# Optimization experiments

Measured on AMD Instinct MI355X. Metric: run time of the kernel, lower is better.

## Reference

```python
import jax, jax.numpy as jnp
import numpy as np

HIDDEN = 4096
NUM_HEADS = 32
NUM_KV_HEADS = 8
HEAD_DIM = 128


def setup_inputs() -> dict:
    key = jax.random.key(0)
    k0, k1, k2, k3, k4 = jax.random.split(key, 5)
    B, S = 1, 2048
    s = 0.02
    return {
        "hidden_states": jax.random.normal(k0, (B, S, HIDDEN), dtype=jnp.float32),
        "Wq": jax.random.normal(k1, (HIDDEN, NUM_HEADS * HEAD_DIM), dtype=jnp.float32) * s,
        "Wk": jax.random.normal(k2, (HIDDEN, NUM_KV_HEADS * HEAD_DIM), dtype=jnp.float32) * s,
        "Wv": jax.random.normal(k3, (HIDDEN, NUM_KV_HEADS * HEAD_DIM), dtype=jnp.float32) * s,
        "Wo": jax.random.normal(k4, (NUM_HEADS * HEAD_DIM, HIDDEN), dtype=jnp.float32) * s,
    }


def reference(hidden_states, Wq, Wk, Wv, Wo):
    B, S, _ = hidden_states.shape
    n_rep = NUM_HEADS // NUM_KV_HEADS
    # Projections -> [B, H, S, D]
    q = (hidden_states @ Wq).reshape(B, S, NUM_HEADS, HEAD_DIM).transpose(0, 2, 1, 3)
    k = (hidden_states @ Wk).reshape(B, S, NUM_KV_HEADS, HEAD_DIM).transpose(0, 2, 1, 3)
    v = (hidden_states @ Wv).reshape(B, S, NUM_KV_HEADS, HEAD_DIM).transpose(0, 2, 1, 3)
    # GQA expansion: repeat_interleave KV heads to match query head count
    k = jnp.repeat(k, n_rep, axis=1)
    v = jnp.repeat(v, n_rep, axis=1)
    scale = HEAD_DIM ** -0.5
    # Full [B, H, S, S] attention scores (faithful to the naive reference)
    scores = jnp.einsum("bhqd,bhkd->bhqk", q, k) * scale
    causal = jnp.tril(jnp.ones((S, S), dtype=bool))
    scores = jnp.where(causal[None, None], scores, jnp.float32(-jnp.inf))
    probs = jax.nn.softmax(scores, axis=-1)
    out = jnp.einsum("bhqk,bhkd->bhqd", probs, v)
    out = out.transpose(0, 2, 1, 3).reshape(B, S, NUM_HEADS * HEAD_DIM)
    return out @ Wo
```

## Files before the change

kernel.cpp:

```cpp
#include <hip/hip_runtime.h>
#include <hip/hip_bf16.h>

typedef __bf16 bf16;
typedef __bf16 bf16x4 __attribute__((ext_vector_type(4)));
typedef __bf16 bf16x8 __attribute__((ext_vector_type(8)));
typedef float  f32x4  __attribute__((ext_vector_type(4)));

#define SEQ  2048
#define HID  4096
#define QKVN 6144

__device__ __forceinline__ void gload_lds16(const void* g, void* l) {
  __builtin_amdgcn_global_load_lds(
      (const __attribute__((address_space(1))) void*)g,
      (__attribute__((address_space(3))) void*)l, 16, 0, 0);
}

__global__ __launch_bounds__(256) void cast_f32_bf16(const float* __restrict__ in,
                                                     bf16* __restrict__ out, int n) {
  int i = (blockIdx.x * 256 + threadIdx.x) * 4;
  int stride = gridDim.x * 256 * 4;
  for (; i < n; i += stride) {
    float4 v = *(const float4*)(in + i);
    bf16x4 o;
    o[0] = (bf16)v.x; o[1] = (bf16)v.y; o[2] = (bf16)v.z; o[3] = (bf16)v.w;
    *(bf16x4*)(out + i) = o;
  }
}

__global__ __launch_bounds__(256) void transpose_cast(const float* __restrict__ W,
                                                      bf16* __restrict__ Wt,
                                                      int N, int roff) {
  __shared__ float tile[64][65];
  int k0 = blockIdx.y * 64;
  int n0 = blockIdx.x * 64;
  int t = threadIdx.x;
  int lr = t >> 4;
  int lc = (t & 15) * 4;
#pragma unroll
  for (int p = 0; p < 4; ++p) {
    int row = p * 16 + lr;
    float4 v = *(const float4*)(W + (size_t)(k0 + row) * N + n0 + lc);
    tile[row][lc] = v.x; tile[row][lc + 1] = v.y;
    tile[row][lc + 2] = v.z; tile[row][lc + 3] = v.w;
  }
  __syncthreads();
#pragma unroll
  for (int p = 0; p < 4; ++p) {
    int n = p * 16 + lr;
    bf16x4 o;
#pragma unroll
    for (int q = 0; q < 4; ++q) o[q] = (bf16)tile[lc + q][n];
    *(bf16x4*)(Wt + (size_t)(roff + n0 + n) * 4096 + k0 + lc) = o;
  }
}

__global__ __launch_bounds__(256) void transpose_v(const bf16* __restrict__ QKV,
                                                   bf16* __restrict__ Vt_g) {
  __shared__ bf16 tile[32][33];
  int s0 = blockIdx.x * 32;
  int d0 = blockIdx.y * 32;
  int g  = blockIdx.z;
  int t = threadIdx.x;
  int r = t >> 5, c = t & 31;
#pragma unroll
  for (int p = 0; p < 4; ++p)
    tile[r + p * 8][c] = QKV[(size_t)(s0 + r + p * 8) * QKVN + 5120 + g * 128 + d0 + c];
  __syncthreads();
#pragma unroll
  for (int p = 0; p < 4; ++p)
    Vt_g[(size_t)(g * 128 + d0 + r + p * 8) * SEQ + s0 + c] = tile[c][r + p * 8];
}

template <typename OUT_T>
__global__ __launch_bounds__(256) void gemm_bt(const bf16* __restrict__ A,
                                               const bf16* __restrict__ Bt,
                                               OUT_T* __restrict__ C,
                                               int K, int ldc) {
  __shared__ __align__(16) bf16 Abuf[128 * 64];
  __shared__ __align__(16) bf16 Bbuf[128 * 64];
  int m0 = blockIdx.y * 128, n0 = blockIdx.x * 128;
  int tid = threadIdx.x, w = tid >> 6, lane = tid & 63;
  int wr = w >> 1, wc = w & 1;
  int l15 = lane & 15, l4 = lane >> 4;
  f32x4 acc[4][4] = {};
  const int nk = K >> 6;
  for (int kt = 0; kt < nk; ++kt) {
    int k0 = kt << 6;
#pragma unroll
    for (int p = 0; p < 4; ++p) {
      int c = p * 256 + tid;
      int row = c >> 3, slot = c & 7;
      int ssl = (slot ^ (row & 7)) << 4;
      gload_lds16((const char*)(A + (size_t)(m0 + row) * K + k0) + ssl, (char*)Abuf + c * 16);
      gload_lds16((const char*)(Bt + (size_t)(n0 + row) * K + k0) + ssl, (char*)Bbuf + c * 16);
    }
    __syncthreads();
    bf16x8 af[4][2], bfr[4][2];
#pragma unroll
    for (int m = 0; m < 4; ++m)
#pragma unroll
      for (int kk = 0; kk < 2; ++kk) {
        int row = wr * 64 + m * 16 + l15;
        af[m][kk] = *(const bf16x8*)((const char*)Abuf + row * 128 +
                                     (((kk * 4 + l4) ^ (row & 7)) << 4));
      }
#pragma unroll
    for (int n = 0; n < 4; ++n)
#pragma unroll
      for (int kk = 0; kk < 2; ++kk) {
        int row = wc * 64 + n * 16 + l15;
        bfr[n][kk] = *(const bf16x8*)((const char*)Bbuf + row * 128 +
                                      (((kk * 4 + l4) ^ (row & 7)) << 4));
      }
#pragma unroll
    for (int kk = 0; kk < 2; ++kk)
#pragma unroll
      for (int m = 0; m < 4; ++m)
#pragma unroll
        for (int n = 0; n < 4; ++n)
          acc[m][n] = __builtin_amdgcn_mfma_f32_16x16x32_bf16(af[m][kk], bfr[n][kk],
                                                              acc[m][n], 0, 0, 0);
    __syncthreads();
  }
#pragma unroll
  for (int m = 0; m < 4; ++m)
#pragma unroll
    for (int n = 0; n < 4; ++n)
#pragma unroll
      for (int i = 0; i < 4; ++i) {
        int row = m0 + wr * 64 + m * 16 + l4 * 4 + i;
        int col = n0 + wc * 64 + n * 16 + l15;
        C[(size_t)row * ldc + col] = (OUT_T)acc[m][n][i];
      }
}

__global__ __launch_bounds__(256, 2) void attn_kernel(const bf16* __restrict__ QKV,
                                                      const bf16* __restrict__ Vt_g,
                                                      bf16* __restrict__ attn) {
  __shared__ __align__(16) bf16 Klds[2][64 * 128];
  __shared__ __align__(16) bf16 Vlds[2][64 * 128];
  __shared__ __align__(16) bf16 Plds[4 * 16 * 64];
  const int bid = blockIdx.x;
  const int g = bid & 7;
  const int rest = bid >> 3;
  const int hi = rest & 3;
  const int pair = rest >> 2;
  const int qb_a = pair, qb_b = 31 - pair;
  const int tid = threadIdx.x, w = tid >> 6, lane = tid & 63;
  const int h = g * 4 + hi;
  const int l15 = lane & 15, l4 = lane >> 4;
  const int wqA = qb_a * 64 + w * 16;
  const int wqB = qb_b * 64 + w * 16;
  const int qcol = h * 128;
  const int kcol = 4096 + g * 128;
  const float scale = 0.08838834764831845f;
  const float LOG2E = 1.4426950408889634f;

  const bf16* Vhead = Vt_g + (size_t)g * 128 * SEQ;

  bf16x8 aqA[4], aqB[4];
#pragma unroll
  for (int kc = 0; kc < 4; ++kc) {
    aqA[kc] = *(const bf16x8*)(QKV + (size_t)(wqA + l15) * QKVN + qcol + kc * 32 + l4 * 8);
    aqB[kc] = *(const bf16x8*)(QKV + (size_t)(wqB + l15) * QKVN + qcol + kc * 32 + l4 * 8);
  }

  f32x4 acc_oA[8] = {}, acc_oB[8] = {};
  float mA[4], lA[4], mB[4], lB[4];
#pragma unroll
  for (int i = 0; i < 4; ++i) { mA[i] = -1e30f; lA[i] = 0.f; mB[i] = -1e30f; lB[i] = 0.f; }

  auto stageKV = [&](int kb, int buf) {
#pragma unroll
    for (int j = 0; j < 4; ++j) {
      int c = tid + (j << 8);
      int krow = c >> 4, kslot = c & 15;
      gload_lds16((const char*)(QKV + (size_t)(kb + krow) * QKVN + kcol) +
                      ((kslot ^ (krow & 7)) << 4),
                  (char*)Klds[buf] + c * 16);
      int vrow = c >> 3, vslot = c & 7;
      gload_lds16(Vhead + (size_t)vrow * SEQ + kb + ((vslot ^ (vrow & 7)) << 3),
                  (char*)Vlds[buf] + c * 16);
    }
  };

  auto compute_block = [&](const bf16x8* aq, f32x4* acc_o, float* mrow, float* lrow,
                           int wq0, int kb, int cur) {
    const char* Kbuf = (const char*)Klds[cur];
    const char* Vbuf = (const char*)Vlds[cur];
    f32x4 accs[4] = {};
    __builtin_amdgcn_s_setprio(1);
#pragma unroll
    for (int n = 0; n < 4; ++n) {
      int row_ = n * 16 + l15;
      int sw = (row_ & 7) << 4;
#pragma unroll
      for (int kc = 0; kc < 4; ++kc) {
        bf16x8 bk = *(const bf16x8*)(Kbuf + row_ * 256 + ((kc * 64 + l4 * 16) ^ sw));
        accs[n] = __builtin_amdgcn_mfma_f32_16x16x32_bf16(aq[kc], bk, accs[n], 0, 0, 0);
      }
    }
    __builtin_amdgcn_s_setprio(0);
    bool needmask = (kb + 64 > wq0);
    float s[4][4];
#pragma unroll
    for (int n = 0; n < 4; ++n)
#pragma unroll
      for (int i = 0; i < 4; ++i) {
        float v = accs[n][i] * scale;
        if (needmask) {
          int ks = kb + n * 16 + l15;
          int qr = wq0 + l4 * 4 + i;
          if (ks > qr) v = -1e30f;
        }
        s[n][i] = v;
      }
    float t4[4];
#pragma unroll
    for (int i = 0; i < 4; ++i) {
      float t = fmaxf(fmaxf(s[0][i], s[1][i]), fmaxf(s[2][i], s[3][i]));
      t = fmaxf(t, __shfl_xor(t, 1));
      t = fmaxf(t, __shfl_xor(t, 2));
      t = fmaxf(t, __shfl_xor(t, 4));
      t = fmaxf(t, __shfl_xor(t, 8));
      t4[i] = t;
    }
    float dm = fmaxf(fmaxf(t4[0] - mrow[0], t4[1] - mrow[1]),
                     fmaxf(t4[2] - mrow[2], t4[3] - mrow[3]));
    if (!__all(dm <= 8.0f)) {
      float fac[4];
#pragma unroll
      for (int i = 0; i < 4; ++i) {
        float mnew = fmaxf(mrow[i], t4[i]);
        fac[i] = exp2f((mrow[i] - mnew) * LOG2E);
        mrow[i] = mnew;
        lrow[i] *= fac[i];
      }
#pragma unroll
      for (int n2 = 0; n2 < 8; ++n2)
#pragma unroll
        for (int i = 0; i < 4; ++i)
          acc_o[n2][i] *= fac[i];
    }
    float ps[4][4];
#pragma unroll
    for (int i = 0; i < 4; ++i) {
      float psum = 0.f;
#pragma unroll
      for (int n = 0; n < 4; ++n) {
        float p = exp2f((s[n][i] - mrow[i]) * LOG2E);
        ps[n][i] = p; psum += p;
      }
      psum += __shfl_xor(psum, 1);
      psum += __shfl_xor(psum, 2);
      psum += __shfl_xor(psum, 4);
      psum += __shfl_xor(psum, 8);
      lrow[i] += psum;
    }
    char* Pw = (char*)Plds + w * 2048;
#pragma unroll
    for (int n = 0; n < 4; ++n)
#pragma unroll
      for (int i = 0; i < 4; ++i) {
        int r = l4 * 4 + i;
        int b = (r * 128 + (n * 16 + l15) * 2) ^ ((r & 7) << 4);
        *(bf16*)(Pw + b) = (bf16)ps[n][i];
      }
    __builtin_amdgcn_sched_barrier(0);
    asm volatile("" ::: "memory");
    bf16x8 pa[2];
#pragma unroll
    for (int kc = 0; kc < 2; ++kc)
      pa[kc] = *(const bf16x8*)(Pw + (l15 * 128 + ((kc * 64 + l4 * 16) ^ ((l15 & 7) << 4))));
    __builtin_amdgcn_s_setprio(1);
#pragma unroll
    for (int n2 = 0; n2 < 8; ++n2) {
      int row_ = n2 * 16 + l15;
      int sw = (row_ & 7) << 4;
#pragma unroll
      for (int kc = 0; kc < 2; ++kc) {
        bf16x8 bv = *(const bf16x8*)(Vbuf + row_ * 128 + ((kc * 64 + l4 * 16) ^ sw));
        acc_o[n2] = __builtin_amdgcn_mfma_f32_16x16x32_bf16(pa[kc], bv, acc_o[n2], 0, 0, 0);
      }
    }
    __builtin_amdgcn_s_setprio(0);
    asm volatile("" ::: "memory");
  };

  stageKV(0, 0);
  __syncthreads();

  int cur = 0;
  for (int kbi = 0; kbi <= qb_b; ++kbi) {
    int kb = kbi * 64;
    if (kbi < qb_b) stageKV(kb + 64, cur ^ 1);
    if (kbi <= qb_a) compute_block(aqA, acc_oA, mA, lA, wqA, kb, cur);
    compute_block(aqB, acc_oB, mB, lB, wqB, kb, cur);
    __syncthreads();
    cur ^= 1;
  }

#pragma unroll
  for (int n2 = 0; n2 < 8; ++n2)
#pragma unroll
    for (int i = 0; i < 4; ++i) {
      int col = qcol + n2 * 16 + l15;
      attn[(size_t)(wqA + l4 * 4 + i) * 4096 + col] = (bf16)(acc_oA[n2][i] / lA[i]);
      attn[(size_t)(wqB + l4 * 4 + i) * 4096 + col] = (bf16)(acc_oB[n2][i] / lB[i]);
    }
}

extern "C" void kernel_launch(void* const* d_in, const int* in_sizes, int n_in,
                              void* d_out, int out_size, void* d_ws, size_t ws_size,
                              hipStream_t stream) {
  const float* X  = (const float*)d_in[0];
  const float* Wq = (const float*)d_in[1];
  const float* Wk = (const float*)d_in[2];
  const float* Wv = (const float*)d_in[3];
  const float* Wo = (const float*)d_in[4];
  float* out = (float*)d_out;

  const size_t XB_OFF  = 0;
  const size_t WT_OFF  = 16777216;
  const size_t VT_OFF  = WT_OFF + 33554432;
  const size_t QKV_OFF = 16777216 + 50331648;
  if (ws_size < (size_t)92274688) return;

  char* ws = (char*)d_ws;
  bf16* Xb    = (bf16*)(ws + XB_OFF);
  bf16* Wt    = (bf16*)(ws + WT_OFF);
  bf16* Vt_g  = (bf16*)(ws + VT_OFF);
  bf16* QKV   = (bf16*)(ws + QKV_OFF);
  bf16* attnb = Xb;

  cast_f32_bf16<<<2048, 256, 0, stream>>>(X, Xb, SEQ * HID);
  transpose_cast<<<dim3(4096 / 64, 4096 / 64), 256, 0, stream>>>(Wq, Wt, 4096, 0);
  transpose_cast<<<dim3(1024 / 64, 4096 / 64), 256, 0, stream>>>(Wk, Wt, 1024, 4096);
  transpose_cast<<<dim3(1024 / 64, 4096 / 64), 256, 0, stream>>>(Wv, Wt, 1024, 5120);
  gemm_bt<bf16><<<dim3(QKVN / 128, SEQ / 128), 256, 0, stream>>>(Xb, Wt, QKV, HID, QKVN);
  transpose_cast<<<dim3(4096 / 64, 4096 / 64), 256, 0, stream>>>(Wo, Wt, 4096, 0);
  transpose_v<<<dim3(SEQ / 32, 4, 8), 256, 0, stream>>>(QKV, Vt_g);
  attn_kernel<<<512, 256, 0, stream>>>(QKV, Vt_g, attnb);
  gemm_bt<float><<<dim3(4096 / 128, SEQ / 128), 256, 0, stream>>>(attnb, Wt, out, HID, 4096);
}
```

Baseline: 379.8 us.

## Rewrite attention inner loop with 32x32 MFMA and register-resident P

Switches the attention kernel from 16x16x32 to 32x32x16 bf16 MFMA and computes S transposed, with K as the A operand. The softmax probabilities are then packed into the PV operand in registers with v_cvt_pk_bf16_f32 and v_permlane32_swap, so the per-wave LDS round trip for P goes away. The work split also changes: each wave now owns 32 query rows of a single q-block, with two waves on the late block and two on the early block, instead of every wave handling 16 rows of both. K/V LDS swizzles are re-laid out to match the new fragments. The risks are more register pressure from the 16-wide accumulators and idle time for the early-block waves once their causal range is done.

```diff
diff --git a/kernel.cpp b/kernel.cpp
--- a/kernel.cpp
+++ b/kernel.cpp
@@ -5,6 +5,8 @@
 typedef __bf16 bf16x4 __attribute__((ext_vector_type(4)));
 typedef __bf16 bf16x8 __attribute__((ext_vector_type(8)));
 typedef float  f32x4  __attribute__((ext_vector_type(4)));
+typedef float  f32x16 __attribute__((ext_vector_type(16)));
+typedef unsigned u32x4 __attribute__((ext_vector_type(4)));
 
 #define SEQ  2048
 #define HID  4096
@@ -14,6 +16,15 @@
   __builtin_amdgcn_global_load_lds(
       (const __attribute__((address_space(1))) void*)g,
       (__attribute__((address_space(3))) void*)l, 16, 0, 0);
+}
+
+__device__ __forceinline__ unsigned cvtpk(float lo, float hi) {
+  unsigned r;
+  asm("v_cvt_pk_bf16_f32 %0, %1, %2" : "=v"(r) : "v"(lo), "v"(hi));
+  return r;
+}
+__device__ __forceinline__ void plswap(unsigned& a, unsigned& b) {
+  asm("v_permlane32_swap_b32 %0, %1" : "+v"(a), "+v"(b));
 }
 
 __global__ __launch_bounds__(256) void cast_f32_bf16(const float* __restrict__ in,
@@ -140,7 +151,6 @@
                                                       bf16* __restrict__ attn) {
   __shared__ __align__(16) bf16 Klds[2][64 * 128];
   __shared__ __align__(16) bf16 Vlds[2][64 * 128];
-  __shared__ __align__(16) bf16 Plds[4 * 16 * 64];
   const int bid = blockIdx.x;
   const int g = bid & 7;
   const int rest = bid >> 3;
@@ -148,144 +158,116 @@
   const int pair = rest >> 2;
   const int qb_a = pair, qb_b = 31 - pair;
   const int tid = threadIdx.x, w = tid >> 6, lane = tid & 63;
-  const int h = g * 4 + hi;
-  const int l15 = lane & 15, l4 = lane >> 4;
-  const int wqA = qb_a * 64 + w * 16;
-  const int wqB = qb_b * 64 + w * 16;
-  const int qcol = h * 128;
+  const int l31 = lane & 31, hh = lane >> 5;
+  const int head = g * 4 + hi;
+  const bool isB = (w < 2);
+  const int myqb = isB ? qb_b : qb_a;
+  const int unit_q0 = myqb * 64 + (w & 1) * 32;
+  const int qcol = head * 128;
   const int kcol = 4096 + g * 128;
   const float scale = 0.08838834764831845f;
   const float LOG2E = 1.4426950408889634f;
 
   const bf16* Vhead = Vt_g + (size_t)g * 128 * SEQ;
 
-  bf16x8 aqA[4], aqB[4];
-#pragma unroll
-  for (int kc = 0; kc < 4; ++kc) {
-    aqA[kc] = *(const bf16x8*)(QKV + (size_t)(wqA + l15) * QKVN + qcol + kc * 32 + l4 * 8);
-    aqB[kc] = *(const bf16x8*)(QKV + (size_t)(wqB + l15) * QKVN + qcol + kc * 32 + l4 * 8);
-  }
-
-  f32x4 acc_oA[8] = {}, acc_oB[8] = {};
-  float mA[4], lA[4], mB[4], lB[4];
-#pragma unroll
-  for (int i = 0; i < 4; ++i) { mA[i] = -1e30f; lA[i] = 0.f; mB[i] = -1e30f; lB[i] = 0.f; }
+  bf16x8 qf[8];
+#pragma unroll
+  for (int db = 0; db < 8; ++db)
+    qf[db] = *(const bf16x8*)(QKV + (size_t)(unit_q0 + l31) * QKVN + qcol +
+                              db * 16 + hh * 8);
+
+  f32x16 acc_o[4] = {};
+  float m_run = -1e30f, l_run = 0.f;
 
   auto stageKV = [&](int kb, int buf) {
 #pragma unroll
     for (int j = 0; j < 4; ++j) {
       int c = tid + (j << 8);
-      int krow = c >> 4, kslot = c & 15;
-      gload_lds16((const char*)(QKV + (size_t)(kb + krow) * QKVN + kcol) +
-                      ((kslot ^ (krow & 7)) << 4),
-                  (char*)Klds[buf] + c * 16);
-      int vrow = c >> 3, vslot = c & 7;
-      gload_lds16(Vhead + (size_t)vrow * SEQ + kb + ((vslot ^ (vrow & 7)) << 3),
-                  (char*)Vlds[buf] + c * 16);
+      int row = c >> 4, s = c & 15;
+      int sl = s ^ (row & 15);
+      gload_lds16((const char*)(QKV + (size_t)(kb + row) * QKVN + kcol) + (sl << 4),
+                  (char*)Klds[buf] + (c << 4));
+      int d = row * 2 + (sl >> 3);
+      int ko = (sl & 7) << 3;
+      gload_lds16(Vhead + (size_t)d * SEQ + kb + ko, (char*)Vlds[buf] + (c << 4));
     }
   };
 
-  auto compute_block = [&](const bf16x8* aq, f32x4* acc_o, float* mrow, float* lrow,
-                           int wq0, int kb, int cur) {
-    const char* Kbuf = (const char*)Klds[cur];
-    const char* Vbuf = (const char*)Vlds[cur];
-    f32x4 accs[4] = {};
+  auto compute_unit = [&](int kb, int cur) {
+    const char* Kb = (const char*)Klds[cur];
+    const char* Vb = (const char*)Vlds[cur];
+    f32x16 s0 = {}, s1 = {};
     __builtin_amdgcn_s_setprio(1);
 #pragma unroll
-    for (int n = 0; n < 4; ++n) {
-      int row_ = n * 16 + l15;
-      int sw = (row_ & 7) << 4;
-#pragma unroll
-      for (int kc = 0; kc < 4; ++kc) {
-        bf16x8 bk = *(const bf16x8*)(Kbuf + row_ * 256 + ((kc * 64 + l4 * 16) ^ sw));
-        accs[n] = __builtin_amdgcn_mfma_f32_16x16x32_bf16(aq[kc], bk, accs[n], 0, 0, 0);
-      }
+    for (int db = 0; db < 8; ++db) {
+      int slot = (db * 2 + hh) ^ (l31 & 15);
+      bf16x8 k0 = *(const bf16x8*)(Kb + l31 * 256 + slot * 16);
+      bf16x8 k1 = *(const bf16x8*)(Kb + (32 + l31) * 256 + slot * 16);
+      s0 = __builtin_amdgcn_mfma_f32_32x32x16_bf16(k0, qf[db], s0, 0, 0, 0);
+      s1 = __builtin_amdgcn_mfma_f32_32x32x16_bf16(k1, qf[db], s1, 0, 0, 0);
     }
     __builtin_amdgcn_s_setprio(0);
-    bool needmask = (kb + 64 > wq0);
-    float s[4][4];
-#pragma unroll
-    for (int n = 0; n < 4; ++n)
-#pragma unroll
-      for (int i = 0; i < 4; ++i) {
-        float v = accs[n][i] * scale;
-        if (needmask) {
-          int ks = kb + n * 16 + l15;
-          int qr = wq0 + l4 * 4 + i;
-          if (ks > qr) v = -1e30f;
-        }
-        s[n][i] = v;
-      }
-    float t4[4];
-#pragma unroll
-    for (int i = 0; i < 4; ++i) {
-      float t = fmaxf(fmaxf(s[0][i], s[1][i]), fmaxf(s[2][i], s[3][i]));
-      t = fmaxf(t, __shfl_xor(t, 1));
-      t = fmaxf(t, __shfl_xor(t, 2));
-      t = fmaxf(t, __shfl_xor(t, 4));
-      t = fmaxf(t, __shfl_xor(t, 8));
-      t4[i] = t;
-    }
-    float dm = fmaxf(fmaxf(t4[0] - mrow[0], t4[1] - mrow[1]),
-                     fmaxf(t4[2] - mrow[2], t4[3] - mrow[3]));
-    if (!__all(dm <= 8.0f)) {
-      float fac[4];
-#pragma unroll
-      for (int i = 0; i < 4; ++i) {
-        float mnew = fmaxf(mrow[i], t4[i]);
-        fac[i] = exp2f((mrow[i] - mnew) * LOG2E);
-        mrow[i] = mnew;
-        lrow[i] *= fac[i];
-      }
-#pragma unroll
-      for (int n2 = 0; n2 < 8; ++n2)
-#pragma unroll
-        for (int i = 0; i < 4; ++i)
-          acc_o[n2][i] *= fac[i];
-    }
-    float ps[4][4];
-#pragma unroll
-    for (int i = 0; i < 4; ++i) {
-      float psum = 0.f;
-#pragma unroll
-      for (int n = 0; n < 4; ++n) {
-        float p = exp2f((s[n][i] - mrow[i]) * LOG2E);
-        ps[n][i] = p; psum += p;
-      }
-      psum += __shfl_xor(psum, 1);
-      psum += __shfl_xor(psum, 2);
-      psum += __shfl_xor(psum, 4);
-      psum += __shfl_xor(psum, 8);
-      lrow[i] += psum;
-    }
-    char* Pw = (char*)Plds + w * 2048;
-#pragma unroll
-    for (int n = 0; n < 4; ++n)
-#pragma unroll
-      for (int i = 0; i < 4; ++i) {
-        int r = l4 * 4 + i;
-        int b = (r * 128 + (n * 16 + l15) * 2) ^ ((r & 7) << 4);
-        *(bf16*)(Pw + b) = (bf16)ps[n][i];
-      }
-    __builtin_amdgcn_sched_barrier(0);
-    asm volatile("" ::: "memory");
-    bf16x8 pa[2];
-#pragma unroll
-    for (int kc = 0; kc < 2; ++kc)
-      pa[kc] = *(const bf16x8*)(Pw + (l15 * 128 + ((kc * 64 + l4 * 16) ^ ((l15 & 7) << 4))));
+    float p0[16], p1[16];
+    const bool needmask = (kb + 64 > unit_q0);
+    const int qg = unit_q0 + l31;
+#pragma unroll
+    for (int r = 0; r < 16; ++r) {
+      float v0 = s0[r] * scale, v1 = s1[r] * scale;
+      if (needmask) {
+        int krow = (r & 3) + 8 * (r >> 2) + 4 * hh;
+        if (kb + krow > qg)      v0 = -1e30f;
+        if (kb + 32 + krow > qg) v1 = -1e30f;
+      }
+      p0[r] = v0; p1[r] = v1;
+    }
+    float t = fmaxf(p0[0], p1[0]);
+#pragma unroll
+    for (int r = 1; r < 16; ++r) t = fmaxf(t, fmaxf(p0[r], p1[r]));
+    t = fmaxf(t, __shfl_xor(t, 32));
+    if (!__all(t - m_run <= 8.0f)) {
+      float mnew = fmaxf(m_run, t);
+      float fac = exp2f((m_run - mnew) * LOG2E);
+      m_run = mnew;
+      l_run *= fac;
+#pragma unroll
+      for (int dt = 0; dt < 4; ++dt)
+#pragma unroll
+        for (int r = 0; r < 16; ++r) acc_o[dt][r] *= fac;
+    }
+    float psum = 0.f;
+#pragma unroll
+    for (int r = 0; r < 16; ++r) {
+      p0[r] = exp2f((p0[r] - m_run) * LOG2E); psum += p0[r];
+      p1[r] = exp2f((p1[r] - m_run) * LOG2E); psum += p1[r];
+    }
+    psum += __shfl_xor(psum, 32);
+    l_run += psum;
+    bf16x8 paf[4];
+#pragma unroll
+    for (int kstep = 0; kstep < 4; ++kstep) {
+      const float* p = (kstep < 2) ? p0 : p1;
+      const int base = (kstep & 1) * 8;
+      unsigned a0 = cvtpk(p[base + 0], p[base + 1]);
+      unsigned b0 = cvtpk(p[base + 4], p[base + 5]);
+      plswap(a0, b0);
+      unsigned a1 = cvtpk(p[base + 2], p[base + 3]);
+      unsigned b1 = cvtpk(p[base + 6], p[base + 7]);
+      plswap(a1, b1);
+      u32x4 pw; pw[0] = a0; pw[1] = a1; pw[2] = b0; pw[3] = b1;
+      paf[kstep] = __builtin_bit_cast(bf16x8, pw);
+    }
     __builtin_amdgcn_s_setprio(1);
 #pragma unroll
-    for (int n2 = 0; n2 < 8; ++n2) {
-      int row_ = n2 * 16 + l15;
-      int sw = (row_ & 7) << 4;
-#pragma unroll
-      for (int kc = 0; kc < 2; ++kc) {
-        bf16x8 bv = *(const bf16x8*)(Vbuf + row_ * 128 + ((kc * 64 + l4 * 16) ^ sw));
-        acc_o[n2] = __builtin_amdgcn_mfma_f32_16x16x32_bf16(pa[kc], bv, acc_o[n2], 0, 0, 0);
+    for (int dt = 0; dt < 4; ++dt) {
+      int vrow = dt * 16 + (l31 >> 1);
+#pragma unroll
+      for (int kstep = 0; kstep < 4; ++kstep) {
+        int slot = ((l31 & 1) * 8 + kstep * 2 + hh) ^ (vrow & 15);
+        bf16x8 vf = *(const bf16x8*)(Vb + vrow * 256 + slot * 16);
+        acc_o[dt] = __builtin_amdgcn_mfma_f32_32x32x16_bf16(vf, paf[kstep], acc_o[dt], 0, 0, 0);
       }
     }
     __builtin_amdgcn_s_setprio(0);
-    asm volatile("" ::: "memory");
   };
 
   stageKV(0, 0);
@@ -295,19 +277,19 @@
   for (int kbi = 0; kbi <= qb_b; ++kbi) {
     int kb = kbi * 64;
     if (kbi < qb_b) stageKV(kb + 64, cur ^ 1);
-    if (kbi <= qb_a) compute_block(aqA, acc_oA, mA, lA, wqA, kb, cur);
-    compute_block(aqB, acc_oB, mB, lB, wqB, kb, cur);
+    if (isB || kbi <= qb_a) compute_unit(kb, cur);
     __syncthreads();
     cur ^= 1;
   }
 
-#pragma unroll
-  for (int n2 = 0; n2 < 8; ++n2)
-#pragma unroll
-    for (int i = 0; i < 4; ++i) {
-      int col = qcol + n2 * 16 + l15;
-      attn[(size_t)(wqA + l4 * 4 + i) * 4096 + col] = (bf16)(acc_oA[n2][i] / lA[i]);
-      attn[(size_t)(wqB + l4 * 4 + i) * 4096 + col] = (bf16)(acc_oB[n2][i] / lB[i]);
+  float inv_l = 1.0f / l_run;
+  bf16* orow = attn + (size_t)(unit_q0 + l31) * 4096 + qcol;
+#pragma unroll
+  for (int dt = 0; dt < 4; ++dt)
+#pragma unroll
+    for (int r = 0; r < 16; ++r) {
+      int d = dt * 32 + (r & 3) + 8 * (r >> 2) + 4 * hh;
+      orow[d] = (bf16)(acc_o[dt][r] * inv_l);
     }
 }
 
```

Result: faster. 369.8 us (-2.6%).
